# Optimization experiments

Hardware: AMD Instinct MI355X
Metric: run time of the kernel (lower is better)

## Reference

```python
import jax, jax.numpy as jnp
import numpy as np

N_HEAD = 16
D_MODEL = 2048
ROPE_BASE = 10000.0


def setup_inputs() -> dict:
    key = jax.random.key(0)
    k1, k2, k3 = jax.random.split(key, 3)
    b, s, d = 2, 2048, D_MODEL
    x = jax.random.normal(k1, (b, s, d), dtype=jnp.float32)
    # torch nn.Linear init scale ~ 1/sqrt(fan_in); keep activations sane
    W_qkv = jax.random.normal(k2, (3 * d, d), dtype=jnp.float32) * (d ** -0.5)
    W_o = jax.random.normal(k3, (d, d), dtype=jnp.float32) * (d ** -0.5)
    return {"x": x, "W_qkv": W_qkv, "W_o": W_o}


def _rotate_half(x):
    x1, x2 = jnp.split(x, 2, axis=-1)
    return jnp.concatenate((-x2, x1), axis=-1)


def _rope_cos_sin(seq_len, d_head, dtype):
    inv_freq = 1.0 / (ROPE_BASE ** (jnp.arange(0, d_head, 2, dtype=jnp.float32) / d_head))
    t = jnp.arange(seq_len, dtype=jnp.float32)
    freqs = jnp.einsum("i,j->ij", t, inv_freq)          # [s, d_head/2]
    emb = jnp.concatenate((freqs, freqs), axis=-1)       # [s, d_head]
    return jnp.cos(emb).astype(dtype)[None, None], jnp.sin(emb).astype(dtype)[None, None]


def reference(x, W_qkv, W_o):
    b, s, d = x.shape
    h = N_HEAD
    dh = d // h
    qkv = x @ W_qkv.T                                    # [b, s, 3d]
    qkv = qkv.reshape(b, s, 3, h, dh)
    q, k, v = (jnp.transpose(qkv[:, :, i], (0, 2, 1, 3)) for i in range(3))  # [b, h, s, dh]
    cos, sin = _rope_cos_sin(s, dh, x.dtype)
    q = q * cos + _rotate_half(q) * sin
    k = k * cos + _rotate_half(k) * sin
    scale = dh ** -0.5
    scores = jnp.einsum("bhqd,bhkd->bhqk", q, k) * scale  # [b, h, s, s]
    causal = jnp.tril(jnp.ones((s, s), dtype=bool))
    scores = jnp.where(causal[None, None], scores, jnp.finfo(scores.dtype).min)
    attn = jax.nn.softmax(scores, axis=-1)
    z = jnp.einsum("bhqk,bhkd->bhqd", attn, v)            # [b, h, s, dh]
    z = jnp.transpose(z, (0, 2, 1, 3)).reshape(b, s, d)
    return z @ W_o.T
```

## Files before the change

### kernel.cpp

```cpp
#include <hip/hip_runtime.h>
#include <stdint.h>
#include <stddef.h>

typedef __attribute__((ext_vector_type(8))) short bf16x8;
typedef __attribute__((ext_vector_type(4))) float f32x4;
typedef __attribute__((ext_vector_type(16))) float f32x16;
typedef __attribute__((ext_vector_type(4))) unsigned int u32x4;

#define AS1 __attribute__((address_space(1)))
#define AS3 __attribute__((address_space(3)))

__device__ __forceinline__ void gll16(const void* g, void* l) {
  __builtin_amdgcn_global_load_lds((const AS1 unsigned int*)g, (AS3 unsigned int*)l, 16, 0, 0);
}

__device__ __forceinline__ uint16_t f2bf(float f) {
  uint32_t u = __builtin_bit_cast(uint32_t, f);
  u += 0x7fffu + ((u >> 16) & 1u);
  return (uint16_t)(u >> 16);
}
__device__ __forceinline__ float bf2f(uint16_t h) {
  uint32_t u = ((uint32_t)h) << 16;
  return __builtin_bit_cast(float, u);
}
__device__ __forceinline__ uint32_t pack2bf(float lo, float hi) {
  return (uint32_t)f2bf(lo) | ((uint32_t)f2bf(hi) << 16);
}

#define BARRIER() do { asm volatile("" ::: "memory"); __builtin_amdgcn_s_barrier(); asm volatile("" ::: "memory"); } while (0)

__global__ void cvt_f32_bf16(const float* __restrict__ in, uint16_t* __restrict__ out, int n8) {
  int i = blockIdx.x * blockDim.x + threadIdx.x;
  if (i >= n8) return;
  float4 a = reinterpret_cast<const float4*>(in)[2 * i];
  float4 b = reinterpret_cast<const float4*>(in)[2 * i + 1];
  union { uint16_t h[8]; u32x4 v; } u;
  u.h[0] = f2bf(a.x); u.h[1] = f2bf(a.y); u.h[2] = f2bf(a.z); u.h[3] = f2bf(a.w);
  u.h[4] = f2bf(b.x); u.h[5] = f2bf(b.y); u.h[6] = f2bf(b.z); u.h[7] = f2bf(b.w);
  reinterpret_cast<u32x4*>(out)[i] = u.v;
}

__global__ void rope_table(float* __restrict__ cosT, float* __restrict__ sinT) {
  int idx = blockIdx.x * blockDim.x + threadIdx.x;
  int s = idx >> 6, i = idx & 63;
  float invf = expf(-(float)i * (9.2103403719761836f / 64.0f));
  float f = (float)s * invf;
  cosT[idx] = cosf(f);
  sinT[idx] = sinf(f);
}

__global__ void rope_apply2(uint16_t* __restrict__ Qb, uint16_t* __restrict__ Kb,
                            const float* __restrict__ cosT, const float* __restrict__ sinT) {
  int idx = blockIdx.x * blockDim.x + threadIdx.x;
  uint16_t* buf = (idx < 4194304) ? Qb : Kb;
  int id = idx & 4194303;
  int i = id & 63;
  int s = (id >> 6) & 2047;
  int bh = id >> 17;
  size_t base = ((size_t)bh * 2048 + s) * 128;
  float x0 = bf2f(buf[base + i]);
  float x1 = bf2f(buf[base + i + 64]);
  float c = cosT[(s << 6) + i], sn = sinT[(s << 6) + i];
  buf[base + i]      = f2bf(x0 * c - x1 * sn);
  buf[base + i + 64] = f2bf(x1 * c + x0 * sn);
}

__global__ __launch_bounds__(256) void gemm_qkv(
    const uint16_t* __restrict__ A,
    const uint16_t* __restrict__ B,
    uint16_t* __restrict__ Qb, uint16_t* __restrict__ Kb, uint16_t* __restrict__ Vt) {
  __shared__ uint16_t Ash[3][128 * 32];
  __shared__ uint16_t Bsh[3][128 * 32];
  const int t = threadIdx.x;
  const int lane = t & 63;
  const int w = t >> 6, wr = w >> 1, wc = w & 1;
  const int fr = lane & 15, fg = lane >> 4, fk = fg * 8;
  const int m0 = blockIdx.x * 128, n0 = blockIdx.y * 128;
  const int K = 2048;
  const int T = K / 32;
  const int c0 = t, c1 = t + 256;

  f32x4 acc[4][4];
#pragma unroll
  for (int i = 0; i < 4; i++)
#pragma unroll
    for (int j = 0; j < 4; j++) acc[i][j] = (f32x4)(0.0f);

#define QKV_STAGE(tile, buf)                                                        \
  {                                                                                 \
    int kt_ = (tile) * 32;                                                          \
    gll16(&A[(size_t)(m0 + (c0 >> 2)) * K + kt_ + (c0 & 3) * 8], &Ash[buf][(c0 & ~63) * 8]); \
    gll16(&A[(size_t)(m0 + (c1 >> 2)) * K + kt_ + (c1 & 3) * 8], &Ash[buf][(c1 & ~63) * 8]); \
    gll16(&B[(size_t)(n0 + (c0 >> 2)) * K + kt_ + (c0 & 3) * 8], &Bsh[buf][(c0 & ~63) * 8]); \
    gll16(&B[(size_t)(n0 + (c1 >> 2)) * K + kt_ + (c1 & 3) * 8], &Bsh[buf][(c1 & ~63) * 8]); \
  }

  QKV_STAGE(0, 0);
  QKV_STAGE(1, 1);
  asm volatile("s_waitcnt vmcnt(4)" ::: "memory");
  BARRIER();

  for (int tl = 0; tl < T; ++tl) {
    const int cur = tl % 3;
    if (tl + 2 < T) QKV_STAGE(tl + 2, (tl + 2) % 3);
    bf16x8 af[4], bfr[4];
#pragma unroll
    for (int mi = 0; mi < 4; mi++) af[mi] = *(const bf16x8*)&Ash[cur][(wr * 64 + mi * 16 + fr) * 32 + fk];
#pragma unroll
    for (int ni = 0; ni < 4; ni++) bfr[ni] = *(const bf16x8*)&Bsh[cur][(wc * 64 + ni * 16 + fr) * 32 + fk];
    __builtin_amdgcn_s_setprio(1);
#pragma unroll
    for (int mi = 0; mi < 4; mi++)
#pragma unroll
      for (int ni = 0; ni < 4; ni++)
        acc[mi][ni] = __builtin_amdgcn_mfma_f32_16x16x32_bf16(af[mi], bfr[ni], acc[mi][ni], 0, 0, 0);
    __builtin_amdgcn_s_setprio(0);
    if (tl + 2 < T) {
      asm volatile("s_waitcnt vmcnt(4)" ::: "memory");
    } else {
      asm volatile("s_waitcnt vmcnt(0)" ::: "memory");
    }
    BARRIER();
  }
#undef QKV_STAGE

#pragma unroll
  for (int mi = 0; mi < 4; mi++) {
#pragma unroll
    for (int ni = 0; ni < 4; ni++) {
      int ng = n0 + wc * 64 + ni * 16 + fr;
      int head = (ng >> 7) & 15, dd = ng & 127;
      if (ng < 4096) {
        uint16_t* dst = (ng < 2048) ? Qb : Kb;
#pragma unroll
        for (int r = 0; r < 4; r++) {
          int mg = m0 + wr * 64 + mi * 16 + fg * 4 + r;
          int b = mg >> 11, si = mg & 2047;
          dst[((size_t)(b * 16 + head) * 2048 + si) * 128 + dd] = f2bf(acc[mi][ni][r]);
        }
      } else {
        uint2 pv = make_uint2(pack2bf(acc[mi][ni][0], acc[mi][ni][1]),
                              pack2bf(acc[mi][ni][2], acc[mi][ni][3]));
        int mg = m0 + wr * 64 + mi * 16 + fg * 4;
        int b = mg >> 11, si = mg & 2047;
        *(uint2*)&Vt[((size_t)(b * 16 + head) * 128 + dd) * 2048 + si] = pv;
      }
    }
  }
}

__global__ __launch_bounds__(256) void gemm_out_k(
    const uint16_t* __restrict__ A,
    const uint16_t* __restrict__ B,
    float* __restrict__ C) {
  __shared__ uint16_t Ash[3][128 * 32];
  __shared__ uint16_t Bsh[3][128 * 32];
  const int t = threadIdx.x;
  const int lane = t & 63;
  const int w = t >> 6, wr = w >> 1, wc = w & 1;
  const int fr = lane & 15, fg = lane >> 4, fk = fg * 8;
  const int m0 = blockIdx.x * 128, n0 = blockIdx.y * 128;
  const int K = 2048;
  const int T = K / 32;
  const int c0 = t, c1 = t + 256;

  f32x4 acc[4][4];
#pragma unroll
  for (int i = 0; i < 4; i++)
#pragma unroll
    for (int j = 0; j < 4; j++) acc[i][j] = (f32x4)(0.0f);

#define OUT_STAGE(tile, buf)                                                        \
  {                                                                                 \
    int kt_ = (tile) * 32;                                                          \
    gll16(&A[(size_t)(m0 + (c0 >> 2)) * K + kt_ + (c0 & 3) * 8], &Ash[buf][(c0 & ~63) * 8]); \
    gll16(&A[(size_t)(m0 + (c1 >> 2)) * K + kt_ + (c1 & 3) * 8], &Ash[buf][(c1 & ~63) * 8]); \
    gll16(&B[(size_t)(n0 + (c0 >> 2)) * K + kt_ + (c0 & 3) * 8], &Bsh[buf][(c0 & ~63) * 8]); \
    gll16(&B[(size_t)(n0 + (c1 >> 2)) * K + kt_ + (c1 & 3) * 8], &Bsh[buf][(c1 & ~63) * 8]); \
  }

  OUT_STAGE(0, 0);
  OUT_STAGE(1, 1);
  asm volatile("s_waitcnt vmcnt(4)" ::: "memory");
  BARRIER();

  for (int tl = 0; tl < T; ++tl) {
    const int cur = tl % 3;
    if (tl + 2 < T) OUT_STAGE(tl + 2, (tl + 2) % 3);
    bf16x8 af[4], bfr[4];
#pragma unroll
    for (int mi = 0; mi < 4; mi++) af[mi] = *(const bf16x8*)&Ash[cur][(wr * 64 + mi * 16 + fr) * 32 + fk];
#pragma unroll
    for (int ni = 0; ni < 4; ni++) bfr[ni] = *(const bf16x8*)&Bsh[cur][(wc * 64 + ni * 16 + fr) * 32 + fk];
    __builtin_amdgcn_s_setprio(1);
#pragma unroll
    for (int mi = 0; mi < 4; mi++)
#pragma unroll
      for (int ni = 0; ni < 4; ni++)
        acc[mi][ni] = __builtin_amdgcn_mfma_f32_16x16x32_bf16(af[mi], bfr[ni], acc[mi][ni], 0, 0, 0);
    __builtin_amdgcn_s_setprio(0);
    if (tl + 2 < T) {
      asm volatile("s_waitcnt vmcnt(4)" ::: "memory");
    } else {
      asm volatile("s_waitcnt vmcnt(0)" ::: "memory");
    }
    BARRIER();
  }
#undef OUT_STAGE

#pragma unroll
  for (int mi = 0; mi < 4; mi++) {
#pragma unroll
    for (int ni = 0; ni < 4; ni++) {
      int ng = n0 + wc * 64 + ni * 16 + fr;
#pragma unroll
      for (int r = 0; r < 4; r++) {
        int mg = m0 + wr * 64 + mi * 16 + fg * 4 + r;
        C[(size_t)mg * 2048 + ng] = acc[mi][ni][r];
      }
    }
  }
}

__device__ __forceinline__ bf16x8 mk_pa(uint32_t p0, uint32_t p1, uint32_t p2, uint32_t p3, int hi) {
  uint32_t x0 = (uint32_t)__shfl_xor((int)p0, 32, 64);
  uint32_t x1 = (uint32_t)__shfl_xor((int)p1, 32, 64);
  uint32_t x2 = (uint32_t)__shfl_xor((int)p2, 32, 64);
  uint32_t x3 = (uint32_t)__shfl_xor((int)p3, 32, 64);
  u32x4 v;
  v[0] = hi ? x2 : p0;
  v[1] = hi ? x3 : p1;
  v[2] = hi ? p2 : x0;
  v[3] = hi ? p3 : x1;
  return __builtin_bit_cast(bf16x8, v);
}

__global__ __launch_bounds__(256, 2) void attn_kernel(
    const uint16_t* __restrict__ Qb, const uint16_t* __restrict__ Kb,
    const uint16_t* __restrict__ Vt, uint16_t* __restrict__ zb) {
  __shared__ uint16_t Ksh[2][64 * 128];
  __shared__ uint16_t Vsh[2][128 * 64];

  const int t = threadIdx.x, lane = t & 63, w = t >> 6;
  const int l31 = lane & 31, hi = lane >> 5;
  const int bx = blockIdx.x, bh = blockIdx.y;
  const int qt = (bh & 16) ? (15 - bx) : bx;
  const int q0 = qt * 128;
  const int qg = q0 + w * 32 + l31;
  const size_t hbase = (size_t)bh * 2048 * 128;
  const float scale2 = 0.08838834764831845f * 1.4426950408889634f;

#define ATT_STAGE(kt, buf)                                                        \
  do {                                                                            \
    const uint16_t* Kg_ = Kb + hbase + (size_t)(kt) * 64 * 128;                   \
    const uint16_t* Vg_ = Vt + hbase + (size_t)(kt) * 64;                         \
    _Pragma("unroll")                                                             \
    for (int i_ = 0; i_ < 4; i_++) {                                              \
      int c_ = t + i_ * 256;                                                      \
      { int row_ = c_ >> 4, cc_ = c_ & 15, scc_ = cc_ ^ (row_ & 7);               \
        gll16(&Kg_[row_ * 128 + scc_ * 8], &Ksh[buf][(c_ & ~63) * 8]); }          \
      { int r_ = c_ >> 3, cc_ = c_ & 7, scc_ = cc_ ^ (r_ & 7);                    \
        gll16(&Vg_[(size_t)r_ * 2048 + scc_ * 8], &Vsh[buf][(c_ & ~63) * 8]); }   \
    }                                                                             \
  } while (0)

  bf16x8 qf[8];
#pragma unroll
  for (int dc = 0; dc < 8; ++dc)
    qf[dc] = *(const bf16x8*)&Qb[hbase + (size_t)qg * 128 + dc * 16 + hi * 8];

  f32x16 oacc[4];
#pragma unroll
  for (int i = 0; i < 4; i++) oacc[i] = (f32x16)(0.0f);
  float mrow = -1e30f, lrow = 0.0f;

  const int ktiles = 2 * qt + 2;
  ATT_STAGE(0, 0);
  asm volatile("s_waitcnt vmcnt(0)" ::: "memory");
  BARRIER();

  for (int kt = 0; kt < ktiles; ++kt) {
    const int cur = kt & 1;
    if (kt + 1 < ktiles) ATT_STAGE(kt + 1, cur ^ 1);

    const int kv_base = kt * 64;
    if (kv_base <= q0 + w * 32 + 31) {
      f32x16 s0 = (f32x16)(0.0f), s1 = (f32x16)(0.0f);
      __builtin_amdgcn_s_setprio(1);
#pragma unroll
      for (int dc = 0; dc < 8; ++dc) {
        int ch = dc * 2 + hi;
        bf16x8 k0 = *(const bf16x8*)&Ksh[cur][l31 * 128 + ((ch ^ (l31 & 7)) * 8)];
        bf16x8 k1 = *(const bf16x8*)&Ksh[cur][(32 + l31) * 128 + ((ch ^ (l31 & 7)) * 8)];
        s0 = __builtin_amdgcn_mfma_f32_32x32x16_bf16(k0, qf[dc], s0, 0, 0, 0);
        s1 = __builtin_amdgcn_mfma_f32_32x32x16_bf16(k1, qf[dc], s1, 0, 0, 0);
      }
      __builtin_amdgcn_s_setprio(0);

      const bool need_mask = (kv_base + 63 > q0 + w * 32);
#pragma unroll
      for (int reg = 0; reg < 16; ++reg) {
        int koff = (reg & 3) + 8 * (reg >> 2) + 4 * hi;
        float a0 = s0[reg] * scale2, a1 = s1[reg] * scale2;
        if (need_mask) {
          if (kv_base + koff > qg) a0 = -1e30f;
          if (kv_base + 32 + koff > qg) a1 = -1e30f;
        }
        s0[reg] = a0; s1[reg] = a1;
      }

      float pmax = -1e30f;
#pragma unroll
      for (int reg = 0; reg < 16; ++reg) pmax = fmaxf(pmax, fmaxf(s0[reg], s1[reg]));
      pmax = fmaxf(pmax, __shfl_xor(pmax, 32, 64));

      bool defer = __all(pmax <= mrow + 8.0f);
      if (!defer) {
        float mnew = fmaxf(mrow, pmax);
        float al = exp2f(mrow - mnew);
        lrow *= al;
#pragma unroll
        for (int reg = 0; reg < 16; ++reg) {
          int src = (reg & 3) + 8 * (reg >> 2) + 4 * hi;
          float ar = __shfl(al, src, 64);
#pragma unroll
          for (int n = 0; n < 4; ++n) oacc[n][reg] *= ar;
        }
        mrow = mnew;
      }

      float ps = 0.0f;
      uint32_t pk0[8], pk1[8];
#pragma unroll
      for (int i = 0; i < 8; ++i) {
        float a = exp2f(s0[2 * i] - mrow), b = exp2f(s0[2 * i + 1] - mrow);
        ps += a + b;
        pk0[i] = pack2bf(a, b);
        float c = exp2f(s1[2 * i] - mrow), d = exp2f(s1[2 * i + 1] - mrow);
        ps += c + d;
        pk1[i] = pack2bf(c, d);
      }
      ps += __shfl_xor(ps, 32, 64);
      lrow += ps;

      bf16x8 pa[4];
      pa[0] = mk_pa(pk0[0], pk0[1], pk0[2], pk0[3], hi);
      pa[1] = mk_pa(pk0[4], pk0[5], pk0[6], pk0[7], hi);
      pa[2] = mk_pa(pk1[0], pk1[1], pk1[2], pk1[3], hi);
      pa[3] = mk_pa(pk1[4], pk1[5], pk1[6], pk1[7], hi);

      __builtin_amdgcn_s_setprio(1);
#pragma unroll
      for (int ksl = 0; ksl < 4; ++ksl) {
        int ch = ksl * 2 + hi;
#pragma unroll
        for (int n = 0; n < 4; ++n) {
          int d = n * 32 + l31;
          bf16x8 vf = *(const bf16x8*)&Vsh[cur][d * 64 + ((ch ^ (d & 7)) * 8)];
          oacc[n] = __builtin_amdgcn_mfma_f32_32x32x16_bf16(pa[ksl], vf, oacc[n], 0, 0, 0);
        }
      }
      __builtin_amdgcn_s_setprio(0);
    }

    asm volatile("s_waitcnt vmcnt(0)" ::: "memory");
    BARRIER();
  }
#undef ATT_STAGE

  const int b = bh >> 4, h = bh & 15;
#pragma unroll
  for (int reg = 0; reg < 16; ++reg) {
    int rloc = (reg & 3) + 8 * (reg >> 2) + 4 * hi;
    float linv = 1.0f / __shfl(lrow, rloc, 64);
    int rowg = q0 + w * 32 + rloc;
    size_t base = ((size_t)b * 2048 + rowg) * 2048 + h * 128 + l31;
#pragma unroll
    for (int n = 0; n < 4; ++n)
      zb[base + n * 32] = f2bf(oacc[n][reg] * linv);
  }
}

extern "C" void kernel_launch(void* const* d_in, const int* in_sizes, int n_in,
                              void* d_out, int out_size, void* d_ws, size_t ws_size,
                              hipStream_t stream) {
  const float* x    = (const float*)d_in[0];
  const float* Wqkv = (const float*)d_in[1];
  const float* Wo   = (const float*)d_in[2];
  float* out = (float*)d_out;
  char* ws = (char*)d_ws;

  uint16_t* Qb    = (uint16_t*)(ws + 0);
  uint16_t* Kb    = (uint16_t*)(ws + 16777216);
  uint16_t* Vt    = (uint16_t*)(ws + 33554432);
  uint16_t* xb    = (uint16_t*)(ws + 50331648);
  uint16_t* zb    = (uint16_t*)(ws + 50331648);
  uint16_t* wqkvb = (uint16_t*)(ws + 67108864);
  uint16_t* wob   = (uint16_t*)(ws + 92274688);
  float*    cosT  = (float*)   (ws + 100663296);
  float*    sinT  = (float*)   (ws + 101187584);

  cvt_f32_bf16<<<4096, 256, 0, stream>>>(x, xb, 8388608 / 8);
  cvt_f32_bf16<<<6144, 256, 0, stream>>>(Wqkv, wqkvb, 12582912 / 8);
  cvt_f32_bf16<<<2048, 256, 0, stream>>>(Wo, wob, 4194304 / 8);
  rope_table<<<512, 256, 0, stream>>>(cosT, sinT);

  gemm_qkv<<<dim3(32, 48), 256, 0, stream>>>(xb, wqkvb, Qb, Kb, Vt);

  rope_apply2<<<32768, 256, 0, stream>>>(Qb, Kb, cosT, sinT);

  attn_kernel<<<dim3(16, 32), 256, 0, stream>>>(Qb, Kb, Vt, zb);

  gemm_out_k<<<dim3(32, 16), 256, 0, stream>>>(zb, wob, out);
}
```

Measured before the change: 312.1 us.

## Rewrite QKV GEMM with 256x256 tiles, swizzled LDS, and interleaved pipeline

The QKV projection GEMM moves from 128x128 tiles with 4 waves and a triple-buffered K=32 pipeline to 256x256 tiles with 8 waves, K=64 steps and double-buffered dynamic shared memory (128 KB). LDS columns are XOR-swizzled to avoid bank conflicts, block indices are remapped for L2 locality, and loads are interleaved with quarter-tile MFMA batches. The aim is higher arithmetic intensity and better latency hiding in the largest GEMM. In exchange it uses more LDS per block, so occupancy is lower, and it adds many extra barriers per K step.

```diff
diff --git a/kernel.cpp b/kernel.cpp
--- a/kernel.cpp
+++ b/kernel.cpp
@@ -65,83 +65,112 @@
   buf[base + i + 64] = f2bf(x1 * c + x0 * sn);
 }
 
-__global__ __launch_bounds__(256) void gemm_qkv(
+__global__ __launch_bounds__(512, 2) void gemm_qkv(
     const uint16_t* __restrict__ A,
     const uint16_t* __restrict__ B,
     uint16_t* __restrict__ Qb, uint16_t* __restrict__ Kb, uint16_t* __restrict__ Vt) {
-  __shared__ uint16_t Ash[3][128 * 32];
-  __shared__ uint16_t Bsh[3][128 * 32];
-  const int t = threadIdx.x;
-  const int lane = t & 63;
-  const int w = t >> 6, wr = w >> 1, wc = w & 1;
-  const int fr = lane & 15, fg = lane >> 4, fk = fg * 8;
-  const int m0 = blockIdx.x * 128, n0 = blockIdx.y * 128;
-  const int K = 2048;
-  const int T = K / 32;
-  const int c0 = t, c1 = t + 256;
-
-  f32x4 acc[4][4];
-#pragma unroll
-  for (int i = 0; i < 4; i++)
+  extern __shared__ uint16_t L[];
+  const int t = threadIdx.x, lane = t & 63, w = t >> 6;
+  const int fr = lane & 15, fg = lane >> 4;
+  const int wm = w >> 2, wn = w & 3;
+  const int flat = blockIdx.y * 16 + blockIdx.x;
+  const int swz = (flat & 7) * 48 + (flat >> 3);
+  const int m0 = (swz & 15) * 256, n0 = (swz >> 4) * 256;
+
+  f32x4 acc[8][4];
+#pragma unroll
+  for (int i = 0; i < 8; i++)
 #pragma unroll
     for (int j = 0; j < 4; j++) acc[i][j] = (f32x4)(0.0f);
 
-#define QKV_STAGE(tile, buf)                                                        \
-  {                                                                                 \
-    int kt_ = (tile) * 32;                                                          \
-    gll16(&A[(size_t)(m0 + (c0 >> 2)) * K + kt_ + (c0 & 3) * 8], &Ash[buf][(c0 & ~63) * 8]); \
-    gll16(&A[(size_t)(m0 + (c1 >> 2)) * K + kt_ + (c1 & 3) * 8], &Ash[buf][(c1 & ~63) * 8]); \
-    gll16(&B[(size_t)(n0 + (c0 >> 2)) * K + kt_ + (c0 & 3) * 8], &Bsh[buf][(c0 & ~63) * 8]); \
-    gll16(&B[(size_t)(n0 + (c1 >> 2)) * K + kt_ + (c1 & 3) * 8], &Bsh[buf][(c1 & ~63) * 8]); \
-  }
-
-  QKV_STAGE(0, 0);
-  QKV_STAGE(1, 1);
-  asm volatile("s_waitcnt vmcnt(4)" ::: "memory");
+#define ST(kt, ab, half)                                                          \
+  do {                                                                            \
+    if ((kt) < 32) {                                                              \
+      const uint16_t* src_ = (ab) ? B : A;                                        \
+      int g0_ = ((ab) ? n0 : m0) + (half) * 128;                                  \
+      uint16_t* dst_ = &L[((((kt) & 1) * 2 + (ab)) * 2 + (half)) * 8192];         \
+      _Pragma("unroll")                                                           \
+      for (int j_ = 0; j_ < 2; ++j_) {                                            \
+        int c_ = t + j_ * 512;                                                    \
+        int row_ = c_ >> 3, cc_ = c_ & 7, scc_ = cc_ ^ (row_ & 7);                \
+        gll16(&src_[(size_t)(g0_ + row_) * 2048 + (kt) * 64 + scc_ * 8],          \
+              &dst_[(c_ & ~63) * 8]);                                             \
+      }                                                                           \
+    }                                                                             \
+  } while (0)
+
+  auto LDA4 = [&](bf16x8 (&af)[8], int buf, int mh) {
+#pragma unroll
+    for (int mi = 0; mi < 4; ++mi)
+#pragma unroll
+      for (int ks = 0; ks < 2; ++ks) {
+        int lr = (mh * 4 + mi) * 16 + fr;
+        int ck = (ks * 4 + fg) ^ (lr & 7);
+        af[mi * 2 + ks] = *(const bf16x8*)&L[((buf * 2 + 0) * 2 + wm) * 8192 + lr * 64 + ck * 8];
+      }
+  };
+  auto LDB2 = [&](bf16x8 (&bfr)[4], int buf, int nh) {
+#pragma unroll
+    for (int ni = 0; ni < 2; ++ni)
+#pragma unroll
+      for (int ks = 0; ks < 2; ++ks) {
+        int rn = (wn & 1) * 64 + (nh * 2 + ni) * 16 + fr;
+        int ck = (ks * 4 + fg) ^ (rn & 7);
+        bfr[ni * 2 + ks] = *(const bf16x8*)&L[((buf * 2 + 1) * 2 + (wn >> 1)) * 8192 + rn * 64 + ck * 8];
+      }
+  };
+  auto MF16 = [&](bf16x8 (&af)[8], bf16x8 (&bfr)[4], int mh, int nh) {
+    __builtin_amdgcn_s_setprio(1);
+#pragma unroll
+    for (int mi = 0; mi < 4; ++mi)
+#pragma unroll
+      for (int ni = 0; ni < 2; ++ni)
+#pragma unroll
+        for (int ks = 0; ks < 2; ++ks)
+          acc[mh * 4 + mi][nh * 2 + ni] = __builtin_amdgcn_mfma_f32_16x16x32_bf16(
+              af[mi * 2 + ks], bfr[ni * 2 + ks], acc[mh * 4 + mi][nh * 2 + ni], 0, 0, 0);
+    __builtin_amdgcn_s_setprio(0);
+  };
+
+  ST(0, 0, 0); ST(0, 0, 1); ST(0, 1, 0); ST(0, 1, 1); ST(1, 0, 0);
+  asm volatile("s_waitcnt vmcnt(2)" ::: "memory");
   BARRIER();
 
-  for (int tl = 0; tl < T; ++tl) {
-    const int cur = tl % 3;
-    if (tl + 2 < T) QKV_STAGE(tl + 2, (tl + 2) % 3);
-    bf16x8 af[4], bfr[4];
-#pragma unroll
-    for (int mi = 0; mi < 4; mi++) af[mi] = *(const bf16x8*)&Ash[cur][(wr * 64 + mi * 16 + fr) * 32 + fk];
-#pragma unroll
-    for (int ni = 0; ni < 4; ni++) bfr[ni] = *(const bf16x8*)&Bsh[cur][(wc * 64 + ni * 16 + fr) * 32 + fk];
-    __builtin_amdgcn_s_setprio(1);
-#pragma unroll
-    for (int mi = 0; mi < 4; mi++)
-#pragma unroll
-      for (int ni = 0; ni < 4; ni++)
-        acc[mi][ni] = __builtin_amdgcn_mfma_f32_16x16x32_bf16(af[mi], bfr[ni], acc[mi][ni], 0, 0, 0);
-    __builtin_amdgcn_s_setprio(0);
-    if (tl + 2 < T) {
-      asm volatile("s_waitcnt vmcnt(4)" ::: "memory");
-    } else {
-      asm volatile("s_waitcnt vmcnt(0)" ::: "memory");
-    }
+  for (int tl = 0; tl < 32; ++tl) {
+    const int buf = tl & 1;
+    bf16x8 af[8], bA[4], bB[4];
+    LDA4(af, buf, 0); LDB2(bA, buf, 0); ST(tl + 1, 0, 1);
+    BARRIER(); MF16(af, bA, 0, 0); BARRIER();
+    LDB2(bB, buf, 1); ST(tl + 1, 1, 0);
+    BARRIER(); MF16(af, bB, 0, 1); BARRIER();
+    LDA4(af, buf, 1); ST(tl + 1, 1, 1);
+    BARRIER(); MF16(af, bA, 1, 0); BARRIER();
+    ST(tl + 2, 0, 0);
+    BARRIER(); MF16(af, bB, 1, 1);
+    if (tl < 30) asm volatile("s_waitcnt vmcnt(2)" ::: "memory");
+    else         asm volatile("s_waitcnt vmcnt(0)" ::: "memory");
     BARRIER();
   }
-#undef QKV_STAGE
-
-#pragma unroll
-  for (int mi = 0; mi < 4; mi++) {
-#pragma unroll
-    for (int ni = 0; ni < 4; ni++) {
-      int ng = n0 + wc * 64 + ni * 16 + fr;
+#undef ST
+
+#pragma unroll
+  for (int mi = 0; mi < 8; ++mi) {
+#pragma unroll
+    for (int ni = 0; ni < 4; ++ni) {
+      int ng = n0 + wn * 64 + ni * 16 + fr;
       int head = (ng >> 7) & 15, dd = ng & 127;
       if (ng < 4096) {
         uint16_t* dst = (ng < 2048) ? Qb : Kb;
 #pragma unroll
         for (int r = 0; r < 4; r++) {
-          int mg = m0 + wr * 64 + mi * 16 + fg * 4 + r;
+          int mg = m0 + wm * 128 + mi * 16 + fg * 4 + r;
           int b = mg >> 11, si = mg & 2047;
           dst[((size_t)(b * 16 + head) * 2048 + si) * 128 + dd] = f2bf(acc[mi][ni][r]);
         }
       } else {
         uint2 pv = make_uint2(pack2bf(acc[mi][ni][0], acc[mi][ni][1]),
                               pack2bf(acc[mi][ni][2], acc[mi][ni][3]));
-        int mg = m0 + wr * 64 + mi * 16 + fg * 4;
+        int mg = m0 + wm * 128 + mi * 16 + fg * 4;
         int b = mg >> 11, si = mg & 2047;
         *(uint2*)&Vt[((size_t)(b * 16 + head) * 128 + dd) * 2048 + si] = pv;
       }
@@ -405,7 +434,7 @@
   cvt_f32_bf16<<<2048, 256, 0, stream>>>(Wo, wob, 4194304 / 8);
   rope_table<<<512, 256, 0, stream>>>(cosT, sinT);
 
-  gemm_qkv<<<dim3(32, 48), 256, 0, stream>>>(xb, wqkvb, Qb, Kb, Vt);
+  gemm_qkv<<<dim3(16, 24), 512, 131072, stream>>>(xb, wqkvb, Qb, Kb, Vt);
 
   rope_apply2<<<32768, 256, 0, stream>>>(Qb, Kb, cosT, sinT);
 
```

New measurement: 306.8 us. Within noise of the previous version (-1.7%).
